# Kernel tuning notes

Measured on AMD Instinct MI355X. Metric: run time of the kernel, lower is better.

The kernel has to match this reference:

```python
import jax, jax.numpy as jnp
import numpy as np

B, N, C = 64, 1700, 256
E_SP, E_TM = 6400, 10000


def gcn_conv(x, W, b, edge_index, num_nodes):
    """PyG GCNConv (normalize=True, add_self_loops=True) on batched [B,N,C] input,
    gathering/scattering along the node axis (node_dim=-2)."""
    row, col = edge_index[0], edge_index[1]
    loops = jnp.arange(num_nodes, dtype=row.dtype)
    row = jnp.concatenate([row, loops])
    col = jnp.concatenate([col, loops])
    w = jnp.ones(row.shape[0], dtype=x.dtype)
    deg = jax.ops.segment_sum(w, col, num_segments=num_nodes)
    dinv = jnp.where(deg > 0, jax.lax.rsqrt(deg), jnp.zeros_like(deg))
    norm = dinv[row] * dinv[col]                      # [E+N]
    h = x @ W                                         # [B,N,Cout]
    msg = h[:, row, :] * norm[None, :, None]          # gather along joints
    out = jnp.zeros((x.shape[0], num_nodes, W.shape[1]), x.dtype)
    out = out.at[:, col, :].add(msg)                  # scatter-add along joints
    return out + b


def setup_inputs() -> dict:
    key = jax.random.key(0)
    ks = jax.random.split(key, 9)
    s = 1.0 / np.sqrt(C)
    return {
        "x": jax.random.normal(ks[0], (B, N, C), jnp.float32),
        "W1": jax.random.uniform(ks[1], (C, C), jnp.float32, -s, s),
        "b1": jnp.zeros((C,), jnp.float32),
        "W2": jax.random.uniform(ks[2], (C, C), jnp.float32, -s, s),
        "b2": jnp.zeros((C,), jnp.float32),
        "W3": jax.random.uniform(ks[3], (C, C), jnp.float32, -s, s),
        "b3": jnp.zeros((C,), jnp.float32),
        "keypoint_line_without_temporal": jax.random.randint(ks[4], (2, E_SP), 0, N, jnp.int32),
        "keypoint_line_with_temporal": jax.random.randint(ks[5], (2, E_TM), 0, N, jnp.int32),
    }


def reference(x, W1, b1, W2, b2, W3, b3,
              keypoint_line_without_temporal, keypoint_line_with_temporal):
    num_nodes = x.shape[1]
    residual = x  # downsample is None -> identity residual
    out = jax.nn.relu(gcn_conv(x, W1, b1, keypoint_line_without_temporal, num_nodes))
    out = jax.nn.relu(gcn_conv(out, W2, b2, keypoint_line_with_temporal, num_nodes))
    out = gcn_conv(out, W3, b3, keypoint_line_without_temporal, num_nodes)
    return jax.nn.relu(out + residual)
```

## Files before the change

### kernel.cpp

```cpp
#include <hip/hip_runtime.h>

#define NNODES 1700
#define CDIM   256

typedef __attribute__((ext_vector_type(8))) short bf16x8;
typedef __attribute__((ext_vector_type(4))) float f32x4;

__device__ inline float bf2f(unsigned h) { return __uint_as_float(h << 16); }
__device__ inline unsigned short f2bf(float f) {
  unsigned u = __float_as_uint(f);
  u = (u + 0x7FFFu + ((u >> 16) & 1u)) >> 16;
  return (unsigned short)u;
}

__device__ inline void async_copy16(const void* gsrc, void* ldst) {
  __builtin_amdgcn_global_load_lds(
      (const __attribute__((address_space(1))) unsigned int*)gsrc,
      (__attribute__((address_space(3))) unsigned int*)ldst,
      16, 0, 0);
}


__global__ void zero_kernel(int* p, int n) {
  int i = blockIdx.x * blockDim.x + threadIdx.x;
  if (i < n) p[i] = 0;
}

__global__ void count_kernel(const int* __restrict__ ei, int E, int* __restrict__ cnt) {
  int i = blockIdx.x * blockDim.x + threadIdx.x;
  if (i < E) atomicAdd(&cnt[ei[E + i]], 1);
}

__global__ void dinv_kernel(const int* __restrict__ cnt, float* __restrict__ dinv, int n) {
  int i = blockIdx.x * blockDim.x + threadIdx.x;
  if (i < n) dinv[i] = rsqrtf((float)(cnt[i] + 1));
}

__global__ __launch_bounds__(1024) void scan_kernel(const int* __restrict__ cnt, int n,
                                                    int* __restrict__ off) {
  __shared__ int s[2048];
  int t = threadIdx.x;
  for (int i = t; i < 2048; i += 1024) s[i] = (i < n) ? (cnt[i] + 1) : 0;
  for (int d = 1; d < 2048; d <<= 1) {
    __syncthreads();
    int idx = (t + 1) * (d << 1) - 1;
    if (idx < 2048) s[idx] += s[idx - d];
  }
  __syncthreads();
  if (t == 0) s[2047] = 0;
  for (int d = 1024; d >= 1; d >>= 1) {
    __syncthreads();
    int idx = (t + 1) * (d << 1) - 1;
    if (idx < 2048) { int tmp = s[idx - d]; s[idx - d] = s[idx]; s[idx] += tmp; }
  }
  __syncthreads();
  for (int i = t; i <= n; i += 1024) off[i] = s[i];
}

__global__ void fill_kernel(const int* __restrict__ ei, int E, int n,
                            const float* __restrict__ dinv, const int* __restrict__ off,
                            int* __restrict__ cursor, int* __restrict__ srcv,
                            float* __restrict__ wv) {
  int i = blockIdx.x * blockDim.x + threadIdx.x;
  if (i >= E + n) return;
  int s, d;
  if (i < E) { s = ei[i]; d = ei[E + i]; } else { s = d = i - E; }
  float w = dinv[s] * dinv[d];
  int p = atomicAdd(&cursor[d], 1);
  int idx = off[d] + p;
  srcv[idx] = s;
  wv[idx] = w;
}

__global__ void transpose_kernel(const float* __restrict__ W,
                                 unsigned short* __restrict__ Wt) {
  int i = blockIdx.x * 256 + threadIdx.x;
  int k = i >> 8, n = i & 255;
  Wt[n * 256 + k] = f2bf(W[i]);
}

__global__ __launch_bounds__(256) void cvt_kernel(const float* __restrict__ x,
                                                  unsigned short* __restrict__ o) {
  size_t i = ((size_t)blockIdx.x * 256 + threadIdx.x) * 8;
  float4 f0 = *(const float4*)(x + i);
  float4 f1 = *(const float4*)(x + i + 4);
  bf16x8 p;
  p[0] = (short)f2bf(f0.x); p[1] = (short)f2bf(f0.y);
  p[2] = (short)f2bf(f0.z); p[3] = (short)f2bf(f0.w);
  p[4] = (short)f2bf(f1.x); p[5] = (short)f2bf(f1.y);
  p[6] = (short)f2bf(f1.z); p[7] = (short)f2bf(f1.w);
  *(bf16x8*)(o + i) = p;
}


template <int K>
__device__ __forceinline__ void kstep(const unsigned short* __restrict__ asrc,
                                      const unsigned short* __restrict__ bsrc,
                                      unsigned short (&As)[3][128 * 32],
                                      unsigned short (&Bs)[3][256 * 32],
                                      int t, int wm, int wn, int lr, int lk,
                                      f32x4 (&acc)[4][4]) {
  if constexpr (K < 7) {
    asm volatile("s_waitcnt vmcnt(3)" ::: "memory");
  } else {
    asm volatile("s_waitcnt vmcnt(0)" ::: "memory");
  }
  __builtin_amdgcn_s_barrier();
  if constexpr (K + 2 < 8) {
    constexpr int S = K + 2;
    async_copy16(asrc + S * 32, &As[S % 3][t * 8]);
    async_copy16(bsrc + S * 32, &Bs[S % 3][t * 8]);
    async_copy16(bsrc + 128 * CDIM + S * 32, &Bs[S % 3][4096 + t * 8]);
  }
  bf16x8 a[4], b[4];
#pragma unroll
  for (int i = 0; i < 4; i++)
    a[i] = *(const bf16x8*)&As[K % 3][(wm + i * 16 + lr) * 32 + lk];
#pragma unroll
  for (int i = 0; i < 4; i++)
    b[i] = *(const bf16x8*)&Bs[K % 3][(wn + i * 16 + lr) * 32 + lk];
#pragma unroll
  for (int mi = 0; mi < 4; mi++)
#pragma unroll
    for (int ni = 0; ni < 4; ni++)
      acc[mi][ni] = __builtin_amdgcn_mfma_f32_16x16x32_bf16(a[mi], b[ni], acc[mi][ni], 0, 0, 0);
}

__global__ __launch_bounds__(512, 4) void gemm_n256(const unsigned short* __restrict__ A,
                                                    const unsigned short* __restrict__ Wt,
                                                    unsigned short* __restrict__ H) {
  __shared__ __align__(16) unsigned short As[3][128 * 32];
  __shared__ __align__(16) unsigned short Bs[3][256 * 32];
  const int m0 = blockIdx.x * 128;
  const int t = threadIdx.x;
  const int lane = t & 63;
  const int w = t >> 6;
  const int wm = (w & 1) * 64;
  const int wn = (w >> 1) * 64;
  const int lr = lane & 15;
  const int lk = (lane >> 4) * 8;

  const unsigned short* asrc = A + (size_t)(m0 + (t >> 2)) * CDIM + (t & 3) * 8;
  const unsigned short* bsrc = Wt + (size_t)(t >> 2) * CDIM + (t & 3) * 8;

  f32x4 acc[4][4] = {};

#pragma unroll
  for (int s = 0; s < 2; s++) {
    async_copy16(asrc + s * 32, &As[s][t * 8]);
    async_copy16(bsrc + s * 32, &Bs[s][t * 8]);
    async_copy16(bsrc + 128 * CDIM + s * 32, &Bs[s][4096 + t * 8]);
  }

  kstep<0>(asrc, bsrc, As, Bs, t, wm, wn, lr, lk, acc);
  kstep<1>(asrc, bsrc, As, Bs, t, wm, wn, lr, lk, acc);
  kstep<2>(asrc, bsrc, As, Bs, t, wm, wn, lr, lk, acc);
  kstep<3>(asrc, bsrc, As, Bs, t, wm, wn, lr, lk, acc);
  kstep<4>(asrc, bsrc, As, Bs, t, wm, wn, lr, lk, acc);
  kstep<5>(asrc, bsrc, As, Bs, t, wm, wn, lr, lk, acc);
  kstep<6>(asrc, bsrc, As, Bs, t, wm, wn, lr, lk, acc);
  kstep<7>(asrc, bsrc, As, Bs, t, wm, wn, lr, lk, acc);

  const int orow = (lane >> 4) * 4;
#pragma unroll
  for (int mi = 0; mi < 4; mi++) {
#pragma unroll
    for (int ni = 0; ni < 4; ni++) {
#pragma unroll
      for (int r = 0; r < 4; r++) {
        int gr = m0 + wm + mi * 16 + orow + r;
        int gc = wn + ni * 16 + lr;
        H[(size_t)gr * CDIM + gc] = f2bf(acc[mi][ni][r]);
      }
    }
  }
}


template <bool FINAL>
__global__ __launch_bounds__(256) void agg_kernel(const unsigned short* __restrict__ H,
                                                  const int* __restrict__ off,
                                                  const int* __restrict__ srcv,
                                                  const float* __restrict__ wv,
                                                  const float* __restrict__ bias,
                                                  const float* __restrict__ resid,
                                                  void* __restrict__ outp) {
  const int n = blockIdx.x;
  const int b = blockIdx.y * 8 + (threadIdx.x >> 5);
  const int c = (threadIdx.x & 31) * 8;
  const int beg = off[n], end = off[n + 1];

  float a0 = 0.f, a1 = 0.f, a2 = 0.f, a3 = 0.f;
  float a4 = 0.f, a5 = 0.f, a6 = 0.f, a7 = 0.f;
  for (int i = beg; i < end; i++) {
    int s = srcv[i];
    float w = wv[i];
    uint4 v = *(const uint4*)(H + ((size_t)b * NNODES + s) * CDIM + c);
    a0 += w * bf2f(v.x & 0xffffu); a1 += w * bf2f(v.x >> 16);
    a2 += w * bf2f(v.y & 0xffffu); a3 += w * bf2f(v.y >> 16);
    a4 += w * bf2f(v.z & 0xffffu); a5 += w * bf2f(v.z >> 16);
    a6 += w * bf2f(v.w & 0xffffu); a7 += w * bf2f(v.w >> 16);
  }
  float4 bv0 = *(const float4*)(bias + c);
  float4 bv1 = *(const float4*)(bias + c + 4);
  a0 += bv0.x; a1 += bv0.y; a2 += bv0.z; a3 += bv0.w;
  a4 += bv1.x; a5 += bv1.y; a6 += bv1.z; a7 += bv1.w;

  const size_t o = ((size_t)b * NNODES + n) * CDIM + c;
  if (FINAL) {
    float4 r0 = *(const float4*)(resid + o);
    float4 r1 = *(const float4*)(resid + o + 4);
    a0 += r0.x; a1 += r0.y; a2 += r0.z; a3 += r0.w;
    a4 += r1.x; a5 += r1.y; a6 += r1.z; a7 += r1.w;
  }
  a0 = fmaxf(a0, 0.f); a1 = fmaxf(a1, 0.f); a2 = fmaxf(a2, 0.f); a3 = fmaxf(a3, 0.f);
  a4 = fmaxf(a4, 0.f); a5 = fmaxf(a5, 0.f); a6 = fmaxf(a6, 0.f); a7 = fmaxf(a7, 0.f);

  if (FINAL) {
    float4 o0, o1;
    o0.x = a0; o0.y = a1; o0.z = a2; o0.w = a3;
    o1.x = a4; o1.y = a5; o1.z = a6; o1.w = a7;
    *(float4*)((float*)outp + o) = o0;
    *(float4*)((float*)outp + o + 4) = o1;
  } else {
    bf16x8 ov;
    ov[0] = (short)f2bf(a0); ov[1] = (short)f2bf(a1);
    ov[2] = (short)f2bf(a2); ov[3] = (short)f2bf(a3);
    ov[4] = (short)f2bf(a4); ov[5] = (short)f2bf(a5);
    ov[6] = (short)f2bf(a6); ov[7] = (short)f2bf(a7);
    *(bf16x8*)((unsigned short*)outp + o) = ov;
  }
}


extern "C" void kernel_launch(void* const* d_in, const int* in_sizes, int n_in,
                              void* d_out, int out_size, void* d_ws, size_t ws_size,
                              hipStream_t stream) {
  const float* x  = (const float*)d_in[0];
  const float* W1 = (const float*)d_in[1];
  const float* b1 = (const float*)d_in[2];
  const float* W2 = (const float*)d_in[3];
  const float* b2 = (const float*)d_in[4];
  const float* W3 = (const float*)d_in[5];
  const float* b3 = (const float*)d_in[6];
  const int* esp = (const int*)d_in[7];
  const int* etm = (const int*)d_in[8];

  const int Esp = in_sizes[7] / 2;
  const int Etm = in_sizes[8] / 2;
  const int B = in_sizes[0] / (NNODES * CDIM);
  const int M = B * NNODES;

  char* ws = (char*)d_ws;
  size_t woff = 0;
  auto alloc = [&](size_t bytes) -> void* {
    void* p = ws + woff;
    woff = (woff + bytes + 255) & ~(size_t)255;
    return p;
  };

  unsigned short* H   = (unsigned short*)alloc((size_t)M * CDIM * 2);
  unsigned short* Act = (unsigned short*)alloc((size_t)M * CDIM * 2);
  unsigned short* Wt  = (unsigned short*)alloc((size_t)3 * CDIM * CDIM * 2);
  int* zero_base = (int*)alloc((size_t)4 * NNODES * sizeof(int));
  int* cnt_sp = zero_base;
  int* cur_sp = zero_base + NNODES;
  int* cnt_tm = zero_base + 2 * NNODES;
  int* cur_tm = zero_base + 3 * NNODES;
  int* off_sp = (int*)alloc((NNODES + 1) * sizeof(int));
  int* off_tm = (int*)alloc((NNODES + 1) * sizeof(int));
  float* dinv_sp = (float*)alloc(NNODES * sizeof(float));
  float* dinv_tm = (float*)alloc(NNODES * sizeof(float));
  int*   src_sp = (int*)alloc((size_t)(Esp + NNODES) * sizeof(int));
  float* wgt_sp = (float*)alloc((size_t)(Esp + NNODES) * sizeof(float));
  int*   src_tm = (int*)alloc((size_t)(Etm + NNODES) * sizeof(int));
  float* wgt_tm = (float*)alloc((size_t)(Etm + NNODES) * sizeof(float));

  zero_kernel<<<(4 * NNODES + 255) / 256, 256, 0, stream>>>(zero_base, 4 * NNODES);
  transpose_kernel<<<256, 256, 0, stream>>>(W1, Wt);
  transpose_kernel<<<256, 256, 0, stream>>>(W2, Wt + CDIM * CDIM);
  transpose_kernel<<<256, 256, 0, stream>>>(W3, Wt + 2 * CDIM * CDIM);
  count_kernel<<<(Esp + 255) / 256, 256, 0, stream>>>(esp, Esp, cnt_sp);
  count_kernel<<<(Etm + 255) / 256, 256, 0, stream>>>(etm, Etm, cnt_tm);
  dinv_kernel<<<(NNODES + 255) / 256, 256, 0, stream>>>(cnt_sp, dinv_sp, NNODES);
  dinv_kernel<<<(NNODES + 255) / 256, 256, 0, stream>>>(cnt_tm, dinv_tm, NNODES);
  scan_kernel<<<1, 1024, 0, stream>>>(cnt_sp, NNODES, off_sp);
  scan_kernel<<<1, 1024, 0, stream>>>(cnt_tm, NNODES, off_tm);
  fill_kernel<<<(Esp + NNODES + 255) / 256, 256, 0, stream>>>(esp, Esp, NNODES, dinv_sp,
                                                              off_sp, cur_sp, src_sp, wgt_sp);
  fill_kernel<<<(Etm + NNODES + 255) / 256, 256, 0, stream>>>(etm, Etm, NNODES, dinv_tm,
                                                              off_tm, cur_tm, src_tm, wgt_tm);

  dim3 ggrid(M / 128);
  dim3 agrid(NNODES, B / 8);

  cvt_kernel<<<(M * CDIM / 8 + 255) / 256, 256, 0, stream>>>(x, Act);

  gemm_n256<<<ggrid, 512, 0, stream>>>(Act, Wt, H);
  agg_kernel<false><<<agrid, 256, 0, stream>>>(H, off_sp, src_sp, wgt_sp, b1, nullptr, Act);
  gemm_n256<<<ggrid, 512, 0, stream>>>(Act, Wt + CDIM * CDIM, H);
  agg_kernel<false><<<agrid, 256, 0, stream>>>(H, off_tm, src_tm, wgt_tm, b2, nullptr, Act);
  gemm_n256<<<ggrid, 512, 0, stream>>>(Act, Wt + 2 * CDIM * CDIM, H);
  agg_kernel<true><<<agrid, 256, 0, stream>>>(H, off_sp, src_sp, wgt_sp, b3, x, d_out);
}
```

Measured before the change: 458.6 us.

## Reorder GCN to aggregate before GEMM and fuse bias/ReLU/residual into GEMM epilogue

Each layer now uses A(XW) = (AX)W, so sparse aggregation runs first and the GEMM epilogue applies bias, ReLU and, in the last layer, the residual. The first aggregation reads fp32 x directly, which removes the separate convert kernel. Preprocessing launches are merged into four kernels, and the aggregation loop handles two edges per iteration to get more loads in flight. The cost is a non-coalesced scattered epilogue that now also reads the residual and writes fp32 output, plus wider fp32 gathers in the first aggregation.

```diff
diff --git a/kernel.cpp b/kernel.cpp
--- a/kernel.cpp
+++ b/kernel.cpp
@@ -21,26 +21,47 @@
 }
 
 
-__global__ void zero_kernel(int* p, int n) {
-  int i = blockIdx.x * blockDim.x + threadIdx.x;
-  if (i < n) p[i] = 0;
-}
-
-__global__ void count_kernel(const int* __restrict__ ei, int E, int* __restrict__ cnt) {
-  int i = blockIdx.x * blockDim.x + threadIdx.x;
-  if (i < E) atomicAdd(&cnt[ei[E + i]], 1);
-}
-
-__global__ void dinv_kernel(const int* __restrict__ cnt, float* __restrict__ dinv, int n) {
-  int i = blockIdx.x * blockDim.x + threadIdx.x;
-  if (i < n) dinv[i] = rsqrtf((float)(cnt[i] + 1));
-}
-
-__global__ __launch_bounds__(1024) void scan_kernel(const int* __restrict__ cnt, int n,
-                                                    int* __restrict__ off) {
+__global__ __launch_bounds__(256) void prep1(const float* __restrict__ W1,
+                                             const float* __restrict__ W2,
+                                             const float* __restrict__ W3,
+                                             unsigned short* __restrict__ Wt,
+                                             int* __restrict__ zb) {
+  int i = blockIdx.x * 256 + threadIdx.x;
+  if (i < 4 * NNODES) zb[i] = 0;
+  if (i < 3 * 65536) {
+    int wsel = i >> 16, e = i & 65535;
+    const float* W = wsel == 0 ? W1 : (wsel == 1 ? W2 : W3);
+    int k = e >> 8, n = e & 255;
+    Wt[(wsel << 16) + n * 256 + k] = f2bf(W[e]);
+  }
+}
+
+__global__ __launch_bounds__(256) void prep2(const int* __restrict__ esp, int Esp,
+                                             const int* __restrict__ etm, int Etm,
+                                             int* __restrict__ cnt_sp,
+                                             int* __restrict__ cnt_tm) {
+  int i = blockIdx.x * 256 + threadIdx.x;
+  if (i < Esp) {
+    atomicAdd(&cnt_sp[esp[Esp + i]], 1);
+  } else {
+    int k = i - Esp;
+    if (k < Etm) atomicAdd(&cnt_tm[etm[Etm + k]], 1);
+  }
+}
+
+__global__ __launch_bounds__(1024) void prep3(const int* __restrict__ cnt_sp,
+                                              float* __restrict__ dinv_sp,
+                                              int* __restrict__ off_sp,
+                                              const int* __restrict__ cnt_tm,
+                                              float* __restrict__ dinv_tm,
+                                              int* __restrict__ off_tm) {
+  const int* cnt = blockIdx.x ? cnt_tm : cnt_sp;
+  float* dinv = blockIdx.x ? dinv_tm : dinv_sp;
+  int* off = blockIdx.x ? off_tm : off_sp;
   __shared__ int s[2048];
   int t = threadIdx.x;
-  for (int i = t; i < 2048; i += 1024) s[i] = (i < n) ? (cnt[i] + 1) : 0;
+  for (int i = t; i < NNODES; i += 1024) dinv[i] = rsqrtf((float)(cnt[i] + 1));
+  for (int i = t; i < 2048; i += 1024) s[i] = (i < NNODES) ? (cnt[i] + 1) : 0;
   for (int d = 1; d < 2048; d <<= 1) {
     __syncthreads();
     int idx = (t + 1) * (d << 1) - 1;
@@ -54,42 +75,89 @@
     if (idx < 2048) { int tmp = s[idx - d]; s[idx - d] = s[idx]; s[idx] += tmp; }
   }
   __syncthreads();
-  for (int i = t; i <= n; i += 1024) off[i] = s[i];
-}
-
-__global__ void fill_kernel(const int* __restrict__ ei, int E, int n,
-                            const float* __restrict__ dinv, const int* __restrict__ off,
-                            int* __restrict__ cursor, int* __restrict__ srcv,
-                            float* __restrict__ wv) {
-  int i = blockIdx.x * blockDim.x + threadIdx.x;
-  if (i >= E + n) return;
-  int s, d;
-  if (i < E) { s = ei[i]; d = ei[E + i]; } else { s = d = i - E; }
-  float w = dinv[s] * dinv[d];
-  int p = atomicAdd(&cursor[d], 1);
-  int idx = off[d] + p;
-  srcv[idx] = s;
-  wv[idx] = w;
-}
-
-__global__ void transpose_kernel(const float* __restrict__ W,
-                                 unsigned short* __restrict__ Wt) {
+  for (int i = t; i <= NNODES; i += 1024) off[i] = s[i];
+}
+
+__global__ __launch_bounds__(256) void prep4(
+    const int* __restrict__ esp, int Esp, const int* __restrict__ etm, int Etm,
+    const float* __restrict__ dinv_sp, const int* __restrict__ off_sp,
+    int* __restrict__ cur_sp, int* __restrict__ src_sp, float* __restrict__ wgt_sp,
+    const float* __restrict__ dinv_tm, const int* __restrict__ off_tm,
+    int* __restrict__ cur_tm, int* __restrict__ src_tm, float* __restrict__ wgt_tm) {
   int i = blockIdx.x * 256 + threadIdx.x;
-  int k = i >> 8, n = i & 255;
-  Wt[n * 256 + k] = f2bf(W[i]);
-}
-
-__global__ __launch_bounds__(256) void cvt_kernel(const float* __restrict__ x,
-                                                  unsigned short* __restrict__ o) {
-  size_t i = ((size_t)blockIdx.x * 256 + threadIdx.x) * 8;
-  float4 f0 = *(const float4*)(x + i);
-  float4 f1 = *(const float4*)(x + i + 4);
-  bf16x8 p;
-  p[0] = (short)f2bf(f0.x); p[1] = (short)f2bf(f0.y);
-  p[2] = (short)f2bf(f0.z); p[3] = (short)f2bf(f0.w);
-  p[4] = (short)f2bf(f1.x); p[5] = (short)f2bf(f1.y);
-  p[6] = (short)f2bf(f1.z); p[7] = (short)f2bf(f1.w);
-  *(bf16x8*)(o + i) = p;
+  const int tot_sp = Esp + NNODES;
+  if (i < tot_sp) {
+    int s, d;
+    if (i < Esp) { s = esp[i]; d = esp[Esp + i]; } else { s = d = i - Esp; }
+    float w = dinv_sp[s] * dinv_sp[d];
+    int p = atomicAdd(&cur_sp[d], 1);
+    int idx = off_sp[d] + p;
+    src_sp[idx] = s; wgt_sp[idx] = w;
+  } else {
+    int k = i - tot_sp;
+    if (k < Etm + NNODES) {
+      int s, d;
+      if (k < Etm) { s = etm[k]; d = etm[Etm + k]; } else { s = d = k - Etm; }
+      float w = dinv_tm[s] * dinv_tm[d];
+      int p = atomicAdd(&cur_tm[d], 1);
+      int idx = off_tm[d] + p;
+      src_tm[idx] = s; wgt_tm[idx] = w;
+    }
+  }
+}
+
+
+template <bool SRCF32>
+__global__ __launch_bounds__(256) void agg_kernel(const void* __restrict__ Xp,
+                                                  const int* __restrict__ off,
+                                                  const int* __restrict__ srcv,
+                                                  const float* __restrict__ wv,
+                                                  unsigned short* __restrict__ Xa) {
+  const int n = blockIdx.x;
+  const int b = blockIdx.y * 8 + (threadIdx.x >> 5);
+  const int c = (threadIdx.x & 31) * 8;
+  const int beg = off[n], end = off[n + 1];
+  const size_t base = (size_t)b * NNODES;
+
+  float a0 = 0.f, a1 = 0.f, a2 = 0.f, a3 = 0.f;
+  float a4 = 0.f, a5 = 0.f, a6 = 0.f, a7 = 0.f;
+  for (int i = beg; i < end; i += 2) {
+    int s0 = srcv[i];
+    float w0 = wv[i];
+    const bool two = (i + 1 < end);
+    int i1 = two ? i + 1 : i;
+    int s1 = srcv[i1];
+    float w1 = two ? wv[i1] : 0.f;
+    if (SRCF32) {
+      const float* X = (const float*)Xp;
+      const float* p0 = X + (base + s0) * CDIM + c;
+      const float* p1 = X + (base + s1) * CDIM + c;
+      float4 u0 = *(const float4*)p0, u1 = *(const float4*)(p0 + 4);
+      float4 v0 = *(const float4*)p1, v1 = *(const float4*)(p1 + 4);
+      a0 += w0 * u0.x + w1 * v0.x; a1 += w0 * u0.y + w1 * v0.y;
+      a2 += w0 * u0.z + w1 * v0.z; a3 += w0 * u0.w + w1 * v0.w;
+      a4 += w0 * u1.x + w1 * v1.x; a5 += w0 * u1.y + w1 * v1.y;
+      a6 += w0 * u1.z + w1 * v1.z; a7 += w0 * u1.w + w1 * v1.w;
+    } else {
+      const unsigned short* X = (const unsigned short*)Xp;
+      uint4 u = *(const uint4*)(X + (base + s0) * CDIM + c);
+      uint4 v = *(const uint4*)(X + (base + s1) * CDIM + c);
+      a0 += w0 * bf2f(u.x & 0xffffu) + w1 * bf2f(v.x & 0xffffu);
+      a1 += w0 * bf2f(u.x >> 16)     + w1 * bf2f(v.x >> 16);
+      a2 += w0 * bf2f(u.y & 0xffffu) + w1 * bf2f(v.y & 0xffffu);
+      a3 += w0 * bf2f(u.y >> 16)     + w1 * bf2f(v.y >> 16);
+      a4 += w0 * bf2f(u.z & 0xffffu) + w1 * bf2f(v.z & 0xffffu);
+      a5 += w0 * bf2f(u.z >> 16)     + w1 * bf2f(v.z >> 16);
+      a6 += w0 * bf2f(u.w & 0xffffu) + w1 * bf2f(v.w & 0xffffu);
+      a7 += w0 * bf2f(u.w >> 16)     + w1 * bf2f(v.w >> 16);
+    }
+  }
+  bf16x8 ov;
+  ov[0] = (short)f2bf(a0); ov[1] = (short)f2bf(a1);
+  ov[2] = (short)f2bf(a2); ov[3] = (short)f2bf(a3);
+  ov[4] = (short)f2bf(a4); ov[5] = (short)f2bf(a5);
+  ov[6] = (short)f2bf(a6); ov[7] = (short)f2bf(a7);
+  *(bf16x8*)(Xa + (base + n) * CDIM + c) = ov;
 }
 
 
@@ -126,9 +194,12 @@
       acc[mi][ni] = __builtin_amdgcn_mfma_f32_16x16x32_bf16(a[mi], b[ni], acc[mi][ni], 0, 0, 0);
 }
 
+template <bool FINAL>
 __global__ __launch_bounds__(512, 4) void gemm_n256(const unsigned short* __restrict__ A,
                                                     const unsigned short* __restrict__ Wt,
-                                                    unsigned short* __restrict__ H) {
+                                                    const float* __restrict__ bias,
+                                                    const float* __restrict__ resid,
+                                                    void* __restrict__ outp) {
   __shared__ __align__(16) unsigned short As[3][128 * 32];
   __shared__ __align__(16) unsigned short Bs[3][256 * 32];
   const int m0 = blockIdx.x * 128;
@@ -161,6 +232,9 @@
   kstep<6>(asrc, bsrc, As, Bs, t, wm, wn, lr, lk, acc);
   kstep<7>(asrc, bsrc, As, Bs, t, wm, wn, lr, lk, acc);
 
+  float bv[4];
+#pragma unroll
+  for (int ni = 0; ni < 4; ni++) bv[ni] = bias[wn + ni * 16 + lr];
   const int orow = (lane >> 4) * 4;
 #pragma unroll
   for (int mi = 0; mi < 4; mi++) {
@@ -168,67 +242,17 @@
     for (int ni = 0; ni < 4; ni++) {
 #pragma unroll
       for (int r = 0; r < 4; r++) {
-        int gr = m0 + wm + mi * 16 + orow + r;
-        int gc = wn + ni * 16 + lr;
-        H[(size_t)gr * CDIM + gc] = f2bf(acc[mi][ni][r]);
+        const size_t gr = (size_t)(m0 + wm + mi * 16 + orow + r);
+        const size_t idx = gr * CDIM + wn + ni * 16 + lr;
+        float v = acc[mi][ni][r] + bv[ni];
+        if (FINAL) {
+          v += resid[idx];
+          ((float*)outp)[idx] = fmaxf(v, 0.f);
+        } else {
+          ((unsigned short*)outp)[idx] = f2bf(fmaxf(v, 0.f));
+        }
       }
     }
-  }
-}
-
-
-template <bool FINAL>
-__global__ __launch_bounds__(256) void agg_kernel(const unsigned short* __restrict__ H,
-                                                  const int* __restrict__ off,
-                                                  const int* __restrict__ srcv,
-                                                  const float* __restrict__ wv,
-                                                  const float* __restrict__ bias,
-                                                  const float* __restrict__ resid,
-                                                  void* __restrict__ outp) {
-  const int n = blockIdx.x;
-  const int b = blockIdx.y * 8 + (threadIdx.x >> 5);
-  const int c = (threadIdx.x & 31) * 8;
-  const int beg = off[n], end = off[n + 1];
-
-  float a0 = 0.f, a1 = 0.f, a2 = 0.f, a3 = 0.f;
-  float a4 = 0.f, a5 = 0.f, a6 = 0.f, a7 = 0.f;
-  for (int i = beg; i < end; i++) {
-    int s = srcv[i];
-    float w = wv[i];
-    uint4 v = *(const uint4*)(H + ((size_t)b * NNODES + s) * CDIM + c);
-    a0 += w * bf2f(v.x & 0xffffu); a1 += w * bf2f(v.x >> 16);
-    a2 += w * bf2f(v.y & 0xffffu); a3 += w * bf2f(v.y >> 16);
-    a4 += w * bf2f(v.z & 0xffffu); a5 += w * bf2f(v.z >> 16);
-    a6 += w * bf2f(v.w & 0xffffu); a7 += w * bf2f(v.w >> 16);
-  }
-  float4 bv0 = *(const float4*)(bias + c);
-  float4 bv1 = *(const float4*)(bias + c + 4);
-  a0 += bv0.x; a1 += bv0.y; a2 += bv0.z; a3 += bv0.w;
-  a4 += bv1.x; a5 += bv1.y; a6 += bv1.z; a7 += bv1.w;
-
-  const size_t o = ((size_t)b * NNODES + n) * CDIM + c;
-  if (FINAL) {
-    float4 r0 = *(const float4*)(resid + o);
-    float4 r1 = *(const float4*)(resid + o + 4);
-    a0 += r0.x; a1 += r0.y; a2 += r0.z; a3 += r0.w;
-    a4 += r1.x; a5 += r1.y; a6 += r1.z; a7 += r1.w;
-  }
-  a0 = fmaxf(a0, 0.f); a1 = fmaxf(a1, 0.f); a2 = fmaxf(a2, 0.f); a3 = fmaxf(a3, 0.f);
-  a4 = fmaxf(a4, 0.f); a5 = fmaxf(a5, 0.f); a6 = fmaxf(a6, 0.f); a7 = fmaxf(a7, 0.f);
-
-  if (FINAL) {
-    float4 o0, o1;
-    o0.x = a0; o0.y = a1; o0.z = a2; o0.w = a3;
-    o1.x = a4; o1.y = a5; o1.z = a6; o1.w = a7;
-    *(float4*)((float*)outp + o) = o0;
-    *(float4*)((float*)outp + o + 4) = o1;
-  } else {
-    bf16x8 ov;
-    ov[0] = (short)f2bf(a0); ov[1] = (short)f2bf(a1);
-    ov[2] = (short)f2bf(a2); ov[3] = (short)f2bf(a3);
-    ov[4] = (short)f2bf(a4); ov[5] = (short)f2bf(a5);
-    ov[6] = (short)f2bf(a6); ov[7] = (short)f2bf(a7);
-    *(bf16x8*)((unsigned short*)outp + o) = ov;
   }
 }
 
@@ -276,30 +300,20 @@
   int*   src_tm = (int*)alloc((size_t)(Etm + NNODES) * sizeof(int));
   float* wgt_tm = (float*)alloc((size_t)(Etm + NNODES) * sizeof(float));
 
-  zero_kernel<<<(4 * NNODES + 255) / 256, 256, 0, stream>>>(zero_base, 4 * NNODES);
-  transpose_kernel<<<256, 256, 0, stream>>>(W1, Wt);
-  transpose_kernel<<<256, 256, 0, stream>>>(W2, Wt + CDIM * CDIM);
-  transpose_kernel<<<256, 256, 0, stream>>>(W3, Wt + 2 * CDIM * CDIM);
-  count_kernel<<<(Esp + 255) / 256, 256, 0, stream>>>(esp, Esp, cnt_sp);
-  count_kernel<<<(Etm + 255) / 256, 256, 0, stream>>>(etm, Etm, cnt_tm);
-  dinv_kernel<<<(NNODES + 255) / 256, 256, 0, stream>>>(cnt_sp, dinv_sp, NNODES);
-  dinv_kernel<<<(NNODES + 255) / 256, 256, 0, stream>>>(cnt_tm, dinv_tm, NNODES);
-  scan_kernel<<<1, 1024, 0, stream>>>(cnt_sp, NNODES, off_sp);
-  scan_kernel<<<1, 1024, 0, stream>>>(cnt_tm, NNODES, off_tm);
-  fill_kernel<<<(Esp + NNODES + 255) / 256, 256, 0, stream>>>(esp, Esp, NNODES, dinv_sp,
-                                                              off_sp, cur_sp, src_sp, wgt_sp);
-  fill_kernel<<<(Etm + NNODES + 255) / 256, 256, 0, stream>>>(etm, Etm, NNODES, dinv_tm,
-                                                              off_tm, cur_tm, src_tm, wgt_tm);
-
+  prep1<<<(3 * 65536 + 255) / 256, 256, 0, stream>>>(W1, W2, W3, Wt, zero_base);
+  prep2<<<(Esp + Etm + 255) / 256, 256, 0, stream>>>(esp, Esp, etm, Etm, cnt_sp, cnt_tm);
+  prep3<<<2, 1024, 0, stream>>>(cnt_sp, dinv_sp, off_sp, cnt_tm, dinv_tm, off_tm);
+  prep4<<<(Esp + Etm + 2 * NNODES + 255) / 256, 256, 0, stream>>>(
+      esp, Esp, etm, Etm, dinv_sp, off_sp, cur_sp, src_sp, wgt_sp,
+      dinv_tm, off_tm, cur_tm, src_tm, wgt_tm);
+
+  dim3 agrid(NNODES, B / 8);
   dim3 ggrid(M / 128);
-  dim3 agrid(NNODES, B / 8);
-
-  cvt_kernel<<<(M * CDIM / 8 + 255) / 256, 256, 0, stream>>>(x, Act);
-
-  gemm_n256<<<ggrid, 512, 0, stream>>>(Act, Wt, H);
-  agg_kernel<false><<<agrid, 256, 0, stream>>>(H, off_sp, src_sp, wgt_sp, b1, nullptr, Act);
-  gemm_n256<<<ggrid, 512, 0, stream>>>(Act, Wt + CDIM * CDIM, H);
-  agg_kernel<false><<<agrid, 256, 0, stream>>>(H, off_tm, src_tm, wgt_tm, b2, nullptr, Act);
-  gemm_n256<<<ggrid, 512, 0, stream>>>(Act, Wt + 2 * CDIM * CDIM, H);
-  agg_kernel<true><<<agrid, 256, 0, stream>>>(H, off_sp, src_sp, wgt_sp, b3, x, d_out);
-}
+
+  agg_kernel<true><<<agrid, 256, 0, stream>>>(x, off_sp, src_sp, wgt_sp, Act);
+  gemm_n256<false><<<ggrid, 512, 0, stream>>>(Act, Wt, b1, nullptr, H);
+  agg_kernel<false><<<agrid, 256, 0, stream>>>(H, off_tm, src_tm, wgt_tm, Act);
+  gemm_n256<false><<<ggrid, 512, 0, stream>>>(Act, Wt + CDIM * CDIM, b2, nullptr, H);
+  agg_kernel<false><<<agrid, 256, 0, stream>>>(H, off_sp, src_sp, wgt_sp, Act);
+  gemm_n256<true><<<ggrid, 512, 0, stream>>>(Act, Wt + 2 * CDIM * CDIM, b3, x, d_out);
+}
```

Result: no change. 465.9 us (+1.6%).
